# Kernel optimization log

Hardware: AMD Instinct MI355X
Metric: run time of the kernel (lower is better)

The kernel has to match this reference:

```python
import jax, jax.numpy as jnp
import numpy as np

W = 4096          # n_wavelengths
S = 4096          # n_spatial_modes
N_KEYS = 1024     # number of stored memories
SHARPNESS = 10.0  # config.retrieval_sharpness


def setup_inputs() -> dict:
    key = jax.random.key(0)
    k = jax.random.split(key, 6)
    return {
        "holo_re": jax.random.normal(k[0], (W, S), dtype=jnp.float32),
        "holo_im": jax.random.normal(k[1], (W, S), dtype=jnp.float32),
        "cue_re": jax.random.normal(k[2], (W, S), dtype=jnp.float32),
        "cue_im": jax.random.normal(k[3], (W, S), dtype=jnp.float32),
        "keys_re": jax.random.normal(k[4], (N_KEYS, W), dtype=jnp.float32),
        "keys_im": jax.random.normal(k[5], (N_KEYS, W), dtype=jnp.float32),
    }


def reference(holo_re, holo_im, cue_re, cue_im, keys_re, keys_im):
    hologram = holo_re + 1j * holo_im      # [W, S] complex64
    cue = cue_re + 1j * cue_im             # [W, S]
    keys = keys_re + 1j * keys_im          # [N, W]
    # noisy_mix = (hologram * cue.conj()).sum(dim=1)
    noisy_mix = jnp.sum(hologram * jnp.conj(cue), axis=1)  # [W]
    # torch.dot does NOT conjugate: plain complex dot per key -> batched matvec
    correlations = jnp.abs(keys @ noisy_mix)               # [N]
    attention = jax.nn.softmax(correlations * SHARPNESS)   # [N] real
    clean_key = attention.astype(keys.dtype) @ keys        # [W] complex
    out = hologram * clean_key[:, None]                    # [W, S] complex
    # return real/imag stacked so the harness compares real arrays
    return jnp.stack([out.real, out.imag])                 # [2, W, S] float32
```

## Files before the change

### kernel.cpp

```cpp
#include <hip/hip_runtime.h>
#include <math.h>

#define WDIM 4096
#define SDIM 4096
#define NKEYS 1024
#define SHARP 10.0f

typedef float v4 __attribute__((ext_vector_type(4)));

__device__ __forceinline__ float wave_reduce_sum(float v) {
#pragma unroll
    for (int off = 32; off > 0; off >>= 1) v += __shfl_down(v, off, 64);
    return v;
}

__global__ __launch_bounds__(256) void k_mix(
    const float* __restrict__ hr, const float* __restrict__ hi,
    const float* __restrict__ cr, const float* __restrict__ ci,
    float* __restrict__ mix_re, float* __restrict__ mix_im) {
    const int w = blockIdx.x;
    const int t = threadIdx.x;
    const int wave = t >> 6, lane = t & 63;
    const size_t base = (size_t)w * SDIM;
    const v4* hr4 = (const v4*)(hr + base);
    const v4* hi4 = (const v4*)(hi + base);
    const v4* cr4 = (const v4*)(cr + base);
    const v4* ci4 = (const v4*)(ci + base);
    v4 a[4], b[4], c[4], d[4];
#pragma unroll
    for (int j = 0; j < 4; ++j) {
        const int idx = t + j * 256;
        a[j] = hr4[idx];
        b[j] = hi4[idx];
        c[j] = __builtin_nontemporal_load(cr4 + idx);
        d[j] = __builtin_nontemporal_load(ci4 + idx);
    }
    float sr = 0.f, si = 0.f;
#pragma unroll
    for (int j = 0; j < 4; ++j) {
        sr += a[j].x * c[j].x + b[j].x * d[j].x;  si += b[j].x * c[j].x - a[j].x * d[j].x;
        sr += a[j].y * c[j].y + b[j].y * d[j].y;  si += b[j].y * c[j].y - a[j].y * d[j].y;
        sr += a[j].z * c[j].z + b[j].z * d[j].z;  si += b[j].z * c[j].z - a[j].z * d[j].z;
        sr += a[j].w * c[j].w + b[j].w * d[j].w;  si += b[j].w * c[j].w - a[j].w * d[j].w;
    }
    sr = wave_reduce_sum(sr);
    si = wave_reduce_sum(si);
    __shared__ float rr[4], ri[4];
    if (lane == 0) { rr[wave] = sr; ri[wave] = si; }
    __syncthreads();
    if (t == 0) {
        mix_re[w] = rr[0] + rr[1] + rr[2] + rr[3];
        mix_im[w] = ri[0] + ri[1] + ri[2] + ri[3];
    }
}

__global__ __launch_bounds__(256) void k_corr(
    const float* __restrict__ kr, const float* __restrict__ ki,
    const float* __restrict__ mr, const float* __restrict__ mi,
    float* __restrict__ corr) {
    const int n = blockIdx.x;
    const int t = threadIdx.x;
    const int wave = t >> 6, lane = t & 63;
    const size_t base = (size_t)n * WDIM;
    const v4* kr4 = (const v4*)(kr + base);
    const v4* ki4 = (const v4*)(ki + base);
    const v4* mr4 = (const v4*)mr;
    const v4* mi4 = (const v4*)mi;
    v4 a[4], b[4], m[4], q[4];
#pragma unroll
    for (int j = 0; j < 4; ++j) {
        const int idx = t + j * 256;
        a[j] = kr4[idx];
        b[j] = ki4[idx];
        m[j] = mr4[idx];
        q[j] = mi4[idx];
    }
    float zr = 0.f, zi = 0.f;
#pragma unroll
    for (int j = 0; j < 4; ++j) {
        zr += a[j].x * m[j].x - b[j].x * q[j].x;  zi += a[j].x * q[j].x + b[j].x * m[j].x;
        zr += a[j].y * m[j].y - b[j].y * q[j].y;  zi += a[j].y * q[j].y + b[j].y * m[j].y;
        zr += a[j].z * m[j].z - b[j].z * q[j].z;  zi += a[j].z * q[j].z + b[j].z * m[j].z;
        zr += a[j].w * m[j].w - b[j].w * q[j].w;  zi += a[j].w * q[j].w + b[j].w * m[j].w;
    }
    zr = wave_reduce_sum(zr);
    zi = wave_reduce_sum(zi);
    __shared__ float rr[4], ri[4];
    if (lane == 0) { rr[wave] = zr; ri[wave] = zi; }
    __syncthreads();
    if (t == 0) {
        const float fr = rr[0] + rr[1] + rr[2] + rr[3];
        const float fi = ri[0] + ri[1] + ri[2] + ri[3];
        corr[n] = sqrtf(fr * fr + fi * fi) * SHARP;
    }
}

__global__ __launch_bounds__(256) void k_clean(
    const float* __restrict__ kr, const float* __restrict__ ki,
    const float* __restrict__ corr,
    float* __restrict__ clean_re, float* __restrict__ clean_im) {
    const int t = threadIdx.x;
    __shared__ float red[256];
    __shared__ float satt[16];

    float v0 = corr[t], v1 = corr[t + 256], v2 = corr[t + 512], v3 = corr[t + 768];
    float m = fmaxf(fmaxf(v0, v1), fmaxf(v2, v3));
    red[t] = m; __syncthreads();
    for (int s = 128; s > 0; s >>= 1) {
        if (t < s) red[t] = fmaxf(red[t], red[t + s]);
        __syncthreads();
    }
    const float mx = red[0];
    __syncthreads();
    float sum = expf(v0 - mx) + expf(v1 - mx) + expf(v2 - mx) + expf(v3 - mx);
    red[t] = sum; __syncthreads();
    for (int s = 128; s > 0; s >>= 1) {
        if (t < s) red[t] += red[t + s];
        __syncthreads();
    }
    const float inv = 1.0f / red[0];
    const int n0 = blockIdx.y * 16;
    if (t < 16) satt[t] = expf(corr[n0 + t] - mx) * inv;
    __syncthreads();

    const int wt = blockIdx.x;
    const int f4 = wt * 256 + t;
    float arx = 0.f, ary = 0.f, arz = 0.f, arw = 0.f;
    float aix = 0.f, aiy = 0.f, aiz = 0.f, aiw = 0.f;
#pragma unroll 1
    for (int jt = 0; jt < 4; ++jt) {
        v4 x[4], y[4]; float a[4];
#pragma unroll
        for (int j = 0; j < 4; ++j) {
            const int n = n0 + jt * 4 + j;
            a[j] = satt[jt * 4 + j];
            x[j] = ((const v4*)(kr + (size_t)n * WDIM))[f4];
            y[j] = ((const v4*)(ki + (size_t)n * WDIM))[f4];
        }
#pragma unroll
        for (int j = 0; j < 4; ++j) {
            arx += a[j] * x[j].x; ary += a[j] * x[j].y; arz += a[j] * x[j].z; arw += a[j] * x[j].w;
            aix += a[j] * y[j].x; aiy += a[j] * y[j].y; aiz += a[j] * y[j].z; aiw += a[j] * y[j].w;
        }
    }
    const int w = f4 * 4;
    atomicAdd(&clean_re[w + 0], arx); atomicAdd(&clean_re[w + 1], ary);
    atomicAdd(&clean_re[w + 2], arz); atomicAdd(&clean_re[w + 3], arw);
    atomicAdd(&clean_im[w + 0], aix); atomicAdd(&clean_im[w + 1], aiy);
    atomicAdd(&clean_im[w + 2], aiz); atomicAdd(&clean_im[w + 3], aiw);
}

__global__ __launch_bounds__(256) void k_out(
    const float* __restrict__ hr, const float* __restrict__ hi,
    const float* __restrict__ cre, const float* __restrict__ cim,
    float* __restrict__ out_re, float* __restrict__ out_im) {
    const int w = blockIdx.x;
    const size_t base = (size_t)w * SDIM;
    const float a = cre[w], b = cim[w];
    const v4* hr4 = (const v4*)(hr + base);
    const v4* hi4 = (const v4*)(hi + base);
    v4* or4 = (v4*)(out_re + base);
    v4* oi4 = (v4*)(out_im + base);
    v4 h[4], g[4];
#pragma unroll
    for (int j = 0; j < 4; ++j) {
        const int i = threadIdx.x + j * 256;
        h[j] = hr4[i];
        g[j] = hi4[i];
    }
#pragma unroll
    for (int j = 0; j < 4; ++j) {
        const int i = threadIdx.x + j * 256;
        v4 orr, oii;
        orr.x = h[j].x * a - g[j].x * b;  oii.x = h[j].x * b + g[j].x * a;
        orr.y = h[j].y * a - g[j].y * b;  oii.y = h[j].y * b + g[j].y * a;
        orr.z = h[j].z * a - g[j].z * b;  oii.z = h[j].z * b + g[j].z * a;
        orr.w = h[j].w * a - g[j].w * b;  oii.w = h[j].w * b + g[j].w * a;
        __builtin_nontemporal_store(orr, or4 + i);
        __builtin_nontemporal_store(oii, oi4 + i);
    }
}

extern "C" void kernel_launch(void* const* d_in, const int* in_sizes, int n_in,
                              void* d_out, int out_size, void* d_ws, size_t ws_size,
                              hipStream_t stream) {
    const float* hr = (const float*)d_in[0];
    const float* hi = (const float*)d_in[1];
    const float* cr = (const float*)d_in[2];
    const float* ci = (const float*)d_in[3];
    const float* kr = (const float*)d_in[4];
    const float* ki = (const float*)d_in[5];

    float* ws = (float*)d_ws;
    float* mix_re = ws;
    float* mix_im = ws + 4096;
    float* corr   = ws + 8192;
    float* cre    = ws + 10240;
    float* cim    = ws + 14336;

    float* out_re = (float*)d_out;
    float* out_im = out_re + (size_t)WDIM * SDIM;

    hipMemsetAsync(cre, 0, 2 * WDIM * sizeof(float), stream);
    k_mix<<<WDIM, 256, 0, stream>>>(hr, hi, cr, ci, mix_re, mix_im);
    k_corr<<<NKEYS, 256, 0, stream>>>(kr, ki, mix_re, mix_im, corr);
    k_clean<<<dim3(4, 64), 256, 0, stream>>>(kr, ki, corr, cre, cim);
    k_out<<<WDIM, 256, 0, stream>>>(hr, hi, cre, cim, out_re, out_im);
}
```

Baseline: 364.9 us.

## Fuse all four stages into one cooperative persistent kernel with grid syncs

Replaces the memset and four separate launches with a single cooperative kernel of 256 blocks of 1024 threads, using grid-wide syncs between the mix, correlation, softmax/clean-key, and output stages. Each block processes the same 16 hologram rows in the mix and output phases, so hologram reads in the output phase might hit in cache. This removes launch gaps and the memset but adds three grid barriers, recomputes the softmax in every block, and loads the hologram nontemporally, which may reduce cache reuse.

```diff
diff --git a/kernel.cpp b/kernel.cpp
--- a/kernel.cpp
+++ b/kernel.cpp
@@ -1,10 +1,15 @@
 #include <hip/hip_runtime.h>
+#include <hip/hip_cooperative_groups.h>
 #include <math.h>
+
+namespace cg = cooperative_groups;
 
 #define WDIM 4096
 #define SDIM 4096
 #define NKEYS 1024
 #define SHARP 10.0f
+#define NBLK 256
+#define BSZ 1024
 
 typedef float v4 __attribute__((ext_vector_type(4)));
 
@@ -14,170 +19,179 @@
     return v;
 }
 
-__global__ __launch_bounds__(256) void k_mix(
+__global__ __launch_bounds__(BSZ) void k_fused(
     const float* __restrict__ hr, const float* __restrict__ hi,
     const float* __restrict__ cr, const float* __restrict__ ci,
-    float* __restrict__ mix_re, float* __restrict__ mix_im) {
-    const int w = blockIdx.x;
+    const float* __restrict__ kr, const float* __restrict__ ki,
+    float* __restrict__ mix_re, float* __restrict__ mix_im,
+    float* __restrict__ corr,
+    float* __restrict__ cre, float* __restrict__ cim,
+    float* __restrict__ out_re, float* __restrict__ out_im) {
+    cg::grid_group grid = cg::this_grid();
+    const int b = blockIdx.x;
     const int t = threadIdx.x;
-    const int wave = t >> 6, lane = t & 63;
-    const size_t base = (size_t)w * SDIM;
-    const v4* hr4 = (const v4*)(hr + base);
-    const v4* hi4 = (const v4*)(hi + base);
-    const v4* cr4 = (const v4*)(cr + base);
-    const v4* ci4 = (const v4*)(ci + base);
-    v4 a[4], b[4], c[4], d[4];
-#pragma unroll
-    for (int j = 0; j < 4; ++j) {
-        const int idx = t + j * 256;
-        a[j] = hr4[idx];
-        b[j] = hi4[idx];
-        c[j] = __builtin_nontemporal_load(cr4 + idx);
-        d[j] = __builtin_nontemporal_load(ci4 + idx);
-    }
-    float sr = 0.f, si = 0.f;
-#pragma unroll
-    for (int j = 0; j < 4; ++j) {
-        sr += a[j].x * c[j].x + b[j].x * d[j].x;  si += b[j].x * c[j].x - a[j].x * d[j].x;
-        sr += a[j].y * c[j].y + b[j].y * d[j].y;  si += b[j].y * c[j].y - a[j].y * d[j].y;
-        sr += a[j].z * c[j].z + b[j].z * d[j].z;  si += b[j].z * c[j].z - a[j].z * d[j].z;
-        sr += a[j].w * c[j].w + b[j].w * d[j].w;  si += b[j].w * c[j].w - a[j].w * d[j].w;
-    }
-    sr = wave_reduce_sum(sr);
-    si = wave_reduce_sum(si);
-    __shared__ float rr[4], ri[4];
-    if (lane == 0) { rr[wave] = sr; ri[wave] = si; }
-    __syncthreads();
-    if (t == 0) {
-        mix_re[w] = rr[0] + rr[1] + rr[2] + rr[3];
-        mix_im[w] = ri[0] + ri[1] + ri[2] + ri[3];
-    }
-}
-
-__global__ __launch_bounds__(256) void k_corr(
-    const float* __restrict__ kr, const float* __restrict__ ki,
-    const float* __restrict__ mr, const float* __restrict__ mi,
-    float* __restrict__ corr) {
-    const int n = blockIdx.x;
-    const int t = threadIdx.x;
-    const int wave = t >> 6, lane = t & 63;
-    const size_t base = (size_t)n * WDIM;
-    const v4* kr4 = (const v4*)(kr + base);
-    const v4* ki4 = (const v4*)(ki + base);
-    const v4* mr4 = (const v4*)mr;
-    const v4* mi4 = (const v4*)mi;
-    v4 a[4], b[4], m[4], q[4];
-#pragma unroll
-    for (int j = 0; j < 4; ++j) {
-        const int idx = t + j * 256;
-        a[j] = kr4[idx];
-        b[j] = ki4[idx];
-        m[j] = mr4[idx];
-        q[j] = mi4[idx];
-    }
-    float zr = 0.f, zi = 0.f;
-#pragma unroll
-    for (int j = 0; j < 4; ++j) {
-        zr += a[j].x * m[j].x - b[j].x * q[j].x;  zi += a[j].x * q[j].x + b[j].x * m[j].x;
-        zr += a[j].y * m[j].y - b[j].y * q[j].y;  zi += a[j].y * q[j].y + b[j].y * m[j].y;
-        zr += a[j].z * m[j].z - b[j].z * q[j].z;  zi += a[j].z * q[j].z + b[j].z * m[j].z;
-        zr += a[j].w * m[j].w - b[j].w * q[j].w;  zi += a[j].w * q[j].w + b[j].w * m[j].w;
-    }
-    zr = wave_reduce_sum(zr);
-    zi = wave_reduce_sum(zi);
-    __shared__ float rr[4], ri[4];
-    if (lane == 0) { rr[wave] = zr; ri[wave] = zi; }
-    __syncthreads();
-    if (t == 0) {
-        const float fr = rr[0] + rr[1] + rr[2] + rr[3];
-        const float fi = ri[0] + ri[1] + ri[2] + ri[3];
-        corr[n] = sqrtf(fr * fr + fi * fi) * SHARP;
-    }
-}
-
-__global__ __launch_bounds__(256) void k_clean(
-    const float* __restrict__ kr, const float* __restrict__ ki,
-    const float* __restrict__ corr,
-    float* __restrict__ clean_re, float* __restrict__ clean_im) {
-    const int t = threadIdx.x;
-    __shared__ float red[256];
-    __shared__ float satt[16];
-
-    float v0 = corr[t], v1 = corr[t + 256], v2 = corr[t + 512], v3 = corr[t + 768];
-    float m = fmaxf(fmaxf(v0, v1), fmaxf(v2, v3));
-    red[t] = m; __syncthreads();
-    for (int s = 128; s > 0; s >>= 1) {
-        if (t < s) red[t] = fmaxf(red[t], red[t + s]);
-        __syncthreads();
-    }
-    const float mx = red[0];
-    __syncthreads();
-    float sum = expf(v0 - mx) + expf(v1 - mx) + expf(v2 - mx) + expf(v3 - mx);
-    red[t] = sum; __syncthreads();
-    for (int s = 128; s > 0; s >>= 1) {
-        if (t < s) red[t] += red[t + s];
-        __syncthreads();
-    }
-    const float inv = 1.0f / red[0];
-    const int n0 = blockIdx.y * 16;
-    if (t < 16) satt[t] = expf(corr[n0 + t] - mx) * inv;
-    __syncthreads();
-
-    const int wt = blockIdx.x;
-    const int f4 = wt * 256 + t;
-    float arx = 0.f, ary = 0.f, arz = 0.f, arw = 0.f;
-    float aix = 0.f, aiy = 0.f, aiz = 0.f, aiw = 0.f;
+    const int g = t >> 8;
+    const int tt = t & 255;
+    const int wv = (t >> 6) & 3;
+    const int lane = t & 63;
+
+    __shared__ float rr[4][4], ri[4][4];
+    __shared__ float red[4][256];
+
+    {
+        const int gid = b * BSZ + t;
+        if (gid < 2 * WDIM) cre[gid] = 0.f;
+    }
+
 #pragma unroll 1
-    for (int jt = 0; jt < 4; ++jt) {
-        v4 x[4], y[4]; float a[4];
-#pragma unroll
-        for (int j = 0; j < 4; ++j) {
-            const int n = n0 + jt * 4 + j;
-            a[j] = satt[jt * 4 + j];
-            x[j] = ((const v4*)(kr + (size_t)n * WDIM))[f4];
-            y[j] = ((const v4*)(ki + (size_t)n * WDIM))[f4];
-        }
-#pragma unroll
-        for (int j = 0; j < 4; ++j) {
-            arx += a[j] * x[j].x; ary += a[j] * x[j].y; arz += a[j] * x[j].z; arw += a[j] * x[j].w;
-            aix += a[j] * y[j].x; aiy += a[j] * y[j].y; aiz += a[j] * y[j].z; aiw += a[j] * y[j].w;
-        }
-    }
-    const int w = f4 * 4;
-    atomicAdd(&clean_re[w + 0], arx); atomicAdd(&clean_re[w + 1], ary);
-    atomicAdd(&clean_re[w + 2], arz); atomicAdd(&clean_re[w + 3], arw);
-    atomicAdd(&clean_im[w + 0], aix); atomicAdd(&clean_im[w + 1], aiy);
-    atomicAdd(&clean_im[w + 2], aiz); atomicAdd(&clean_im[w + 3], aiw);
-}
-
-__global__ __launch_bounds__(256) void k_out(
-    const float* __restrict__ hr, const float* __restrict__ hi,
-    const float* __restrict__ cre, const float* __restrict__ cim,
-    float* __restrict__ out_re, float* __restrict__ out_im) {
-    const int w = blockIdx.x;
-    const size_t base = (size_t)w * SDIM;
-    const float a = cre[w], b = cim[w];
-    const v4* hr4 = (const v4*)(hr + base);
-    const v4* hi4 = (const v4*)(hi + base);
-    v4* or4 = (v4*)(out_re + base);
-    v4* oi4 = (v4*)(out_im + base);
-    v4 h[4], g[4];
-#pragma unroll
-    for (int j = 0; j < 4; ++j) {
-        const int i = threadIdx.x + j * 256;
-        h[j] = hr4[i];
-        g[j] = hi4[i];
-    }
-#pragma unroll
-    for (int j = 0; j < 4; ++j) {
-        const int i = threadIdx.x + j * 256;
-        v4 orr, oii;
-        orr.x = h[j].x * a - g[j].x * b;  oii.x = h[j].x * b + g[j].x * a;
-        orr.y = h[j].y * a - g[j].y * b;  oii.y = h[j].y * b + g[j].y * a;
-        orr.z = h[j].z * a - g[j].z * b;  oii.z = h[j].z * b + g[j].z * a;
-        orr.w = h[j].w * a - g[j].w * b;  oii.w = h[j].w * b + g[j].w * a;
-        __builtin_nontemporal_store(orr, or4 + i);
-        __builtin_nontemporal_store(oii, oi4 + i);
+    for (int r = 0; r < 4; ++r) {
+        const int w = b * 16 + r * 4 + g;
+        const size_t base = (size_t)w * SDIM;
+        const v4* hr4 = (const v4*)(hr + base);
+        const v4* hi4 = (const v4*)(hi + base);
+        const v4* cr4 = (const v4*)(cr + base);
+        const v4* ci4 = (const v4*)(ci + base);
+        v4 A[4], B[4], C[4], D[4];
+#pragma unroll
+        for (int j = 0; j < 4; ++j) {
+            const int idx = tt + j * 256;
+            C[j] = __builtin_nontemporal_load(cr4 + idx);
+            D[j] = __builtin_nontemporal_load(ci4 + idx);
+        }
+#pragma unroll
+        for (int j = 0; j < 4; ++j) {
+            const int idx = tt + j * 256;
+            A[j] = __builtin_nontemporal_load(hr4 + idx);
+            B[j] = __builtin_nontemporal_load(hi4 + idx);
+        }
+        float sr = 0.f, si = 0.f;
+#pragma unroll
+        for (int j = 0; j < 4; ++j) {
+            sr += A[j].x * C[j].x + B[j].x * D[j].x;  si += B[j].x * C[j].x - A[j].x * D[j].x;
+            sr += A[j].y * C[j].y + B[j].y * D[j].y;  si += B[j].y * C[j].y - A[j].y * D[j].y;
+            sr += A[j].z * C[j].z + B[j].z * D[j].z;  si += B[j].z * C[j].z - A[j].z * D[j].z;
+            sr += A[j].w * C[j].w + B[j].w * D[j].w;  si += B[j].w * C[j].w - A[j].w * D[j].w;
+        }
+        sr = wave_reduce_sum(sr);
+        si = wave_reduce_sum(si);
+        if (lane == 0) { rr[g][wv] = sr; ri[g][wv] = si; }
+        __syncthreads();
+        if (tt == 0) {
+            mix_re[w] = rr[g][0] + rr[g][1] + rr[g][2] + rr[g][3];
+            mix_im[w] = ri[g][0] + ri[g][1] + ri[g][2] + ri[g][3];
+        }
+        __syncthreads();
+    }
+
+    grid.sync();
+
+    {
+        const int n = b * 4 + g;
+        const size_t base = (size_t)n * WDIM;
+        const v4* kr4 = (const v4*)(kr + base);
+        const v4* ki4 = (const v4*)(ki + base);
+        const v4* mr4 = (const v4*)mix_re;
+        const v4* mi4 = (const v4*)mix_im;
+        v4 A[4], B[4], M[4], Q[4];
+#pragma unroll
+        for (int j = 0; j < 4; ++j) {
+            const int idx = tt + j * 256;
+            A[j] = kr4[idx];
+            B[j] = ki4[idx];
+            M[j] = mr4[idx];
+            Q[j] = mi4[idx];
+        }
+        float zr = 0.f, zi = 0.f;
+#pragma unroll
+        for (int j = 0; j < 4; ++j) {
+            zr += A[j].x * M[j].x - B[j].x * Q[j].x;  zi += A[j].x * Q[j].x + B[j].x * M[j].x;
+            zr += A[j].y * M[j].y - B[j].y * Q[j].y;  zi += A[j].y * Q[j].y + B[j].y * M[j].y;
+            zr += A[j].z * M[j].z - B[j].z * Q[j].z;  zi += A[j].z * Q[j].z + B[j].z * M[j].z;
+            zr += A[j].w * M[j].w - B[j].w * Q[j].w;  zi += A[j].w * Q[j].w + B[j].w * M[j].w;
+        }
+        zr = wave_reduce_sum(zr);
+        zi = wave_reduce_sum(zi);
+        if (lane == 0) { rr[g][wv] = zr; ri[g][wv] = zi; }
+        __syncthreads();
+        if (tt == 0) {
+            const float fr = rr[g][0] + rr[g][1] + rr[g][2] + rr[g][3];
+            const float fi = ri[g][0] + ri[g][1] + ri[g][2] + ri[g][3];
+            corr[n] = sqrtf(fr * fr + fi * fi) * SHARP;
+        }
+    }
+
+    grid.sync();
+
+    {
+        const float v0 = corr[tt], v1 = corr[tt + 256],
+                    v2 = corr[tt + 512], v3 = corr[tt + 768];
+        float mloc = fmaxf(fmaxf(v0, v1), fmaxf(v2, v3));
+        red[g][tt] = mloc; __syncthreads();
+        for (int s = 128; s > 0; s >>= 1) {
+            if (tt < s) red[g][tt] = fmaxf(red[g][tt], red[g][tt + s]);
+            __syncthreads();
+        }
+        const float mx = red[g][0];
+        __syncthreads();
+        float sum = expf(v0 - mx) + expf(v1 - mx) + expf(v2 - mx) + expf(v3 - mx);
+        red[g][tt] = sum; __syncthreads();
+        for (int s = 128; s > 0; s >>= 1) {
+            if (tt < s) red[g][tt] += red[g][tt + s];
+            __syncthreads();
+        }
+        const float inv = 1.0f / red[g][0];
+
+        const int G = b * 4 + g;
+        const int wt = G >> 8;
+        const int n0 = (G & 255) * 4;
+        const int f4 = wt * 256 + tt;
+        float arx = 0.f, ary = 0.f, arz = 0.f, arw = 0.f;
+        float aix = 0.f, aiy = 0.f, aiz = 0.f, aiw = 0.f;
+#pragma unroll
+        for (int j = 0; j < 4; ++j) {
+            const int n = n0 + j;
+            const float a = expf(corr[n] - mx) * inv;
+            const v4 x = ((const v4*)(kr + (size_t)n * WDIM))[f4];
+            const v4 y = ((const v4*)(ki + (size_t)n * WDIM))[f4];
+            arx += a * x.x; ary += a * x.y; arz += a * x.z; arw += a * x.w;
+            aix += a * y.x; aiy += a * y.y; aiz += a * y.z; aiw += a * y.w;
+        }
+        const int w = f4 * 4;
+        atomicAdd(&cre[w + 0], arx); atomicAdd(&cre[w + 1], ary);
+        atomicAdd(&cre[w + 2], arz); atomicAdd(&cre[w + 3], arw);
+        atomicAdd(&cim[w + 0], aix); atomicAdd(&cim[w + 1], aiy);
+        atomicAdd(&cim[w + 2], aiz); atomicAdd(&cim[w + 3], aiw);
+    }
+
+    grid.sync();
+
+#pragma unroll 1
+    for (int r = 0; r < 4; ++r) {
+        const int w = b * 16 + r * 4 + g;
+        const size_t base = (size_t)w * SDIM;
+        const float a = cre[w], bc = cim[w];
+        const v4* hr4 = (const v4*)(hr + base);
+        const v4* hi4 = (const v4*)(hi + base);
+        v4* or4 = (v4*)(out_re + base);
+        v4* oi4 = (v4*)(out_im + base);
+        v4 H[4], G4[4];
+#pragma unroll
+        for (int j = 0; j < 4; ++j) {
+            const int i = tt + j * 256;
+            H[j] = __builtin_nontemporal_load(hr4 + i);
+            G4[j] = __builtin_nontemporal_load(hi4 + i);
+        }
+#pragma unroll
+        for (int j = 0; j < 4; ++j) {
+            const int i = tt + j * 256;
+            v4 orr, oii;
+            orr.x = H[j].x * a - G4[j].x * bc;  oii.x = H[j].x * bc + G4[j].x * a;
+            orr.y = H[j].y * a - G4[j].y * bc;  oii.y = H[j].y * bc + G4[j].y * a;
+            orr.z = H[j].z * a - G4[j].z * bc;  oii.z = H[j].z * bc + G4[j].z * a;
+            orr.w = H[j].w * a - G4[j].w * bc;  oii.w = H[j].w * bc + G4[j].w * a;
+            __builtin_nontemporal_store(orr, or4 + i);
+            __builtin_nontemporal_store(oii, oi4 + i);
+        }
     }
 }
 
@@ -201,9 +215,13 @@
     float* out_re = (float*)d_out;
     float* out_im = out_re + (size_t)WDIM * SDIM;
 
-    hipMemsetAsync(cre, 0, 2 * WDIM * sizeof(float), stream);
-    k_mix<<<WDIM, 256, 0, stream>>>(hr, hi, cr, ci, mix_re, mix_im);
-    k_corr<<<NKEYS, 256, 0, stream>>>(kr, ki, mix_re, mix_im, corr);
-    k_clean<<<dim3(4, 64), 256, 0, stream>>>(kr, ki, corr, cre, cim);
-    k_out<<<WDIM, 256, 0, stream>>>(hr, hi, cre, cim, out_re, out_im);
+    void* args[] = {
+        (void*)&hr, (void*)&hi, (void*)&cr, (void*)&ci,
+        (void*)&kr, (void*)&ki,
+        (void*)&mix_re, (void*)&mix_im, (void*)&corr,
+        (void*)&cre, (void*)&cim,
+        (void*)&out_re, (void*)&out_im,
+    };
+    hipLaunchCooperativeKernel((void*)k_fused, dim3(NBLK), dim3(BSZ),
+                               args, 0, stream);
 }
```

Result: slower. 479.5 us (+31.4%).
